# Performance work log

Hardware: AMD Instinct MI355X
Metric: run time of the kernel (lower is better)

## Reference

```python
import jax, jax.numpy as jnp
import numpy as np

B, N, D_IN = 256, 64, 128   # batch, n_agents, input_dim
H0, H1, H2 = 256, 256, 64   # rnn_hidden_dim[0], [1], [2]


def setup_inputs() -> dict:
    key = jax.random.key(0)
    ks = jax.random.split(key, 14)
    s = 0.05
    return {
        "obs": jax.random.normal(ks[0], (B, N, D_IN), dtype=jnp.float32),
        "W_enc": jax.random.normal(ks[1], (H0, D_IN), dtype=jnp.float32) * s,
        "b_enc": jax.random.normal(ks[2], (H0,), dtype=jnp.float32) * s,
        "W_obs": jax.random.normal(ks[3], (H0, H0), dtype=jnp.float32) * s,
        "b_obs": jax.random.normal(ks[4], (H0,), dtype=jnp.float32) * s,
        "W_ih": jax.random.normal(ks[5], (3 * H0, H0), dtype=jnp.float32) * s,
        "b_ih": jax.random.normal(ks[6], (3 * H0,), dtype=jnp.float32) * s,
        "W_hh": jax.random.normal(ks[7], (3 * H0, H0), dtype=jnp.float32) * s,
        "b_hh": jax.random.normal(ks[8], (3 * H0,), dtype=jnp.float32) * s,
        "W_val": jax.random.normal(ks[9], (H1, H0), dtype=jnp.float32) * s,
        "b_val": jax.random.normal(ks[10], (H1,), dtype=jnp.float32) * s,
        "W_dec": jax.random.normal(ks[11], (H2, H1), dtype=jnp.float32) * s,
        "b_dec": jax.random.normal(ks[12], (H2,), dtype=jnp.float32) * s,
    }


def reference(obs, W_enc, b_enc, W_obs, b_obs, W_ih, b_ih, W_hh, b_hh,
              W_val, b_val, W_dec, b_dec):
    # encoding + f_obs  -> h: [B, N, H0]
    x = jax.nn.relu(jnp.einsum("bnd,hd->bnh", obs, W_enc) + b_enc)
    h = jnp.einsum("bnh,gh->bng", x, W_obs) + b_obs

    # comm: mean over other agents. Original masks self and divides by N
    # (mean over dim of size N with self zeroed) => (sum_all - self) / N.
    c = (jnp.sum(h, axis=1, keepdims=True) - h) / N  # [B, N, H0]

    # GRUCell(input=c, hidden=h), PyTorch gate ordering r, z, n
    gi = jnp.einsum("bnh,gh->bng", c, W_ih) + b_ih   # [B, N, 3*H0]
    gh = jnp.einsum("bnh,gh->bng", h, W_hh) + b_hh
    gi_r, gi_z, gi_n = jnp.split(gi, 3, axis=-1)
    gh_r, gh_z, gh_n = jnp.split(gh, 3, axis=-1)
    r = jax.nn.sigmoid(gi_r + gh_r)
    z = jax.nn.sigmoid(gi_z + gh_z)
    n = jnp.tanh(gi_n + r * gh_n)
    h = (1.0 - z) * n + z * h  # [B, N, H0]

    # value head + decoding; seq_len=1 squeezed -> [B, N, H2]
    v = jnp.einsum("bnh,vh->bnv", h, W_val) + b_val
    out = jnp.einsum("bnv,ov->bno", v, W_dec) + b_dec
    return out
```

## Files before the change

### kernel.cpp

```cpp
#include <hip/hip_runtime.h>
#include <hip/hip_bf16.h>
#include <math.h>


typedef __bf16  bf16x8 __attribute__((ext_vector_type(8)));
typedef float   f32x4  __attribute__((ext_vector_type(4)));

#define DIN 128
#define H0  256
#define SW  264
#define SWO 136
#define LOG2E 1.44269504088896f

#define O_WENC 0
#define O_WOBS 32768
#define O_WIH  98304
#define O_WHH  294912
#define W_TOT4 491520
#define O_WVD  491520
#define BVD_BYTE 1015808

__device__ __forceinline__ f32x4 mfma16(bf16x8 a, bf16x8 b, f32x4 c) {
    return __builtin_amdgcn_mfma_f32_16x16x32_bf16(a, b, c, 0, 0, 0);
}
__device__ __forceinline__ float bf2f(__hip_bfloat16 x) { return __bfloat162float(x); }
__device__ __forceinline__ __hip_bfloat16 f2bf(float x) { return __float2bfloat16(x); }
__device__ __forceinline__ float fsigmoid(float x) {
    float e = __builtin_amdgcn_exp2f(-LOG2E * x);
    return __builtin_amdgcn_rcpf(1.0f + e);
}
__device__ __forceinline__ float ftanh(float x) {
    float e = __builtin_amdgcn_exp2f(2.0f * LOG2E * x);
    return 1.0f - 2.0f * __builtin_amdgcn_rcpf(1.0f + e);
}
__device__ __forceinline__ bf16x8 w8(const __hip_bfloat16* p, int idx) {
    return *(const bf16x8*)(p + idx);
}

__global__ __launch_bounds__(256) void prep_kernel(
    const float* __restrict__ W_enc, const float* __restrict__ W_obs,
    const float* __restrict__ W_ih,  const float* __restrict__ W_hh,
    __hip_bfloat16* __restrict__ ws)
{
    const int i = (blockIdx.x * 256 + threadIdx.x) * 8;
    if (i >= W_TOT4) return;
    const float* src; int off;
    if      (i < O_WOBS) { src = W_enc; off = O_WENC; }
    else if (i < O_WIH)  { src = W_obs; off = O_WOBS; }
    else if (i < O_WHH)  { src = W_ih;  off = O_WIH;  }
    else                 { src = W_hh;  off = O_WHH;  }
    const float* f = src + (i - off);
    f32x4 a = *(const f32x4*)f;
    f32x4 b = *(const f32x4*)(f + 4);
    bf16x8 v;
    #pragma unroll
    for (int j = 0; j < 4; j++) { v[j] = (__bf16)a[j]; v[j + 4] = (__bf16)b[j]; }
    *(bf16x8*)(ws + i) = v;
}

__global__ __launch_bounds__(256) void wvd_kernel(
    const float* __restrict__ W_dec, const float* __restrict__ W_val,
    const float* __restrict__ b_val, const float* __restrict__ b_dec,
    __hip_bfloat16* __restrict__ wvd, float* __restrict__ bvd)
{
    const int o = blockIdx.x;
    const int h = threadIdx.x;
    float acc = 0.0f;
    for (int v = 0; v < 256; v++)
        acc += W_dec[o * 256 + v] * W_val[v * 256 + h];
    wvd[o * 256 + h] = f2bf(acc);
    if (h == 0) {
        float b = b_dec[o];
        for (int v = 0; v < 256; v++) b += W_dec[o * 256 + v] * b_val[v];
        bvd[o] = b;
    }
}

__global__ __launch_bounds__(512, 1) void commnet_v8(
    const __hip_bfloat16* __restrict__ ws, const float* __restrict__ bvd,
    const float* __restrict__ b_enc, const float* __restrict__ b_obs,
    const float* __restrict__ b_ih,  const float* __restrict__ b_hh,
    const float* __restrict__ obs,   float* __restrict__ out)
{
    __shared__ __align__(16) __hip_bfloat16 T0[64 * SW];
    __shared__ __align__(16) __hip_bfloat16 T1[64 * SW];

    const __hip_bfloat16* W_enc = ws + O_WENC;
    const __hip_bfloat16* W_obs = ws + O_WOBS;
    const __hip_bfloat16* W_ih  = ws + O_WIH;
    const __hip_bfloat16* W_hh  = ws + O_WHH;
    const __hip_bfloat16* W_vd  = ws + O_WVD;

    const int tid  = threadIdx.x;
    const int wave = tid >> 6;
    const int lane = tid & 63;
    const int quad = lane >> 4;
    const int lc   = lane & 15;
    const int row0 = blockIdx.x * 64;
    const int ko16 = quad * 8;

    #pragma unroll
    for (int j = 0; j < 2; j++) {
        const int u = tid + j * 512;
        const int r = u >> 4, c = (u & 15) << 3;
        const float* src = obs + (row0 + r) * DIN + c;
        f32x4 a = *(const f32x4*)src;
        f32x4 b = *(const f32x4*)(src + 4);
        bf16x8 v;
        #pragma unroll
        for (int q = 0; q < 4; q++) { v[q] = (__bf16)a[q]; v[q + 4] = (__bf16)b[q]; }
        *(bf16x8*)&T1[r * SWO + c] = v;
    }
    __syncthreads();

    #pragma unroll
    for (int cp = 0; cp < 2; cp++) {
        const int n = (wave + 8 * cp) * 16 + lc;
        const float bias = b_enc[n];
        f32x4 acc[4] = {};
        bf16x8 wc = w8(W_enc, n * DIN + ko16);
        #pragma unroll
        for (int k0 = 0; k0 < DIN; k0 += 32) {
            bf16x8 wn = w8(W_enc, n * DIN + (((k0 + 32) & (DIN - 1)) + ko16));
            const int kk = k0 + ko16;
            #pragma unroll
            for (int rt = 0; rt < 4; rt++) {
                bf16x8 a = *(const bf16x8*)&T1[(rt * 16 + lc) * SWO + kk];
                acc[rt] = mfma16(a, wc, acc[rt]);
            }
            wc = wn;
        }
        #pragma unroll
        for (int rt = 0; rt < 4; rt++)
            #pragma unroll
            for (int i = 0; i < 4; i++)
                T0[(rt * 16 + quad * 4 + i) * SW + n] = f2bf(fmaxf(acc[rt][i] + bias, 0.0f));
    }
    __syncthreads();

    #pragma unroll
    for (int cp = 0; cp < 2; cp++) {
        const int n = (wave + 8 * cp) * 16 + lc;
        const float bias = b_obs[n];
        f32x4 acc[4] = {};
        bf16x8 wc = w8(W_obs, n * H0 + ko16);
        #pragma unroll 2
        for (int k0 = 0; k0 < H0; k0 += 32) {
            bf16x8 wn = w8(W_obs, n * H0 + (((k0 + 32) & (H0 - 1)) + ko16));
            const int kk = k0 + ko16;
            #pragma unroll
            for (int rt = 0; rt < 4; rt++) {
                bf16x8 a = *(const bf16x8*)&T0[(rt * 16 + lc) * SW + kk];
                acc[rt] = mfma16(a, wc, acc[rt]);
            }
            wc = wn;
        }
        #pragma unroll
        for (int rt = 0; rt < 4; rt++)
            #pragma unroll
            for (int i = 0; i < 4; i++)
                T1[(rt * 16 + quad * 4 + i) * SW + n] = f2bf(acc[rt][i] + bias);
    }
    __syncthreads();

    #pragma unroll
    for (int cp = 0; cp < 2; cp++) {
        const int n = (wave + 8 * cp) * 16 + lc;
        const float bir = b_ih[n], biz = b_ih[n + 256], bin = b_ih[n + 512];
        const float bhr = b_hh[n], bhz = b_hh[n + 256], bhn = b_hh[n + 512];
        f32x4 gir[4] = {}, giz[4] = {}, gin[4] = {};
        f32x4 ghr[4] = {}, ghz[4] = {}, ghn[4] = {};
        bf16x8 c0 = w8(W_ih, (n      ) * H0 + ko16);
        bf16x8 c1 = w8(W_ih, (n + 256) * H0 + ko16);
        bf16x8 c2 = w8(W_ih, (n + 512) * H0 + ko16);
        bf16x8 c3 = w8(W_hh, (n      ) * H0 + ko16);
        bf16x8 c4 = w8(W_hh, (n + 256) * H0 + ko16);
        bf16x8 c5 = w8(W_hh, (n + 512) * H0 + ko16);
        #pragma unroll 2
        for (int k0 = 0; k0 < H0; k0 += 32) {
            const int kn = ((k0 + 32) & (H0 - 1)) + ko16;
            bf16x8 d0 = w8(W_ih, (n      ) * H0 + kn);
            bf16x8 d1 = w8(W_ih, (n + 256) * H0 + kn);
            bf16x8 d2 = w8(W_ih, (n + 512) * H0 + kn);
            bf16x8 d3 = w8(W_hh, (n      ) * H0 + kn);
            bf16x8 d4 = w8(W_hh, (n + 256) * H0 + kn);
            bf16x8 d5 = w8(W_hh, (n + 512) * H0 + kn);
            const int kk = k0 + ko16;
            #pragma unroll
            for (int rt = 0; rt < 4; rt++) {
                bf16x8 aH = *(const bf16x8*)&T1[(rt * 16 + lc) * SW + kk];
                gir[rt] = mfma16(aH, c0, gir[rt]);
                giz[rt] = mfma16(aH, c1, giz[rt]);
                gin[rt] = mfma16(aH, c2, gin[rt]);
                ghr[rt] = mfma16(aH, c3, ghr[rt]);
                ghz[rt] = mfma16(aH, c4, ghz[rt]);
                ghn[rt] = mfma16(aH, c5, ghn[rt]);
            }
            c0 = d0; c1 = d1; c2 = d2; c3 = d3; c4 = d4; c5 = d5;
        }
        float Sr = 0.0f, Sz = 0.0f, Sn = 0.0f;
        #pragma unroll
        for (int rt = 0; rt < 4; rt++)
            #pragma unroll
            for (int i = 0; i < 4; i++) {
                Sr += gir[rt][i]; Sz += giz[rt][i]; Sn += gin[rt][i];
            }
        Sr += __shfl_xor(Sr, 16); Sr += __shfl_xor(Sr, 32);
        Sz += __shfl_xor(Sz, 16); Sz += __shfl_xor(Sz, 32);
        Sn += __shfl_xor(Sn, 16); Sn += __shfl_xor(Sn, 32);
        #pragma unroll
        for (int rt = 0; rt < 4; rt++)
            #pragma unroll
            for (int i = 0; i < 4; i++) {
                const int row = rt * 16 + quad * 4 + i;
                const float gi_r = (Sr - gir[rt][i]) * (1.0f / 64.0f) + bir;
                const float gi_z = (Sz - giz[rt][i]) * (1.0f / 64.0f) + biz;
                const float gi_n = (Sn - gin[rt][i]) * (1.0f / 64.0f) + bin;
                const float r  = fsigmoid(gi_r + ghr[rt][i] + bhr);
                const float z  = fsigmoid(gi_z + ghz[rt][i] + bhz);
                const float nn = ftanh(gi_n + r * (ghn[rt][i] + bhn));
                const float h  = bf2f(T1[row * SW + n]);
                T0[row * SW + n] = f2bf((1.0f - z) * nn + z * h);
            }
    }
    __syncthreads();

    {
        const int ct  = wave & 3;
        const int rtb = (wave >> 2) * 2;
        const int n   = ct * 16 + lc;
        const float bias = bvd[n];
        f32x4 acc[2] = {};
        bf16x8 wc = w8(W_vd, n * H0 + ko16);
        #pragma unroll
        for (int k0 = 0; k0 < H0; k0 += 32) {
            bf16x8 wn = w8(W_vd, n * H0 + (((k0 + 32) & (H0 - 1)) + ko16));
            const int kk = k0 + ko16;
            #pragma unroll
            for (int j = 0; j < 2; j++) {
                bf16x8 a = *(const bf16x8*)&T0[((rtb + j) * 16 + lc) * SW + kk];
                acc[j] = mfma16(a, wc, acc[j]);
            }
            wc = wn;
        }
        #pragma unroll
        for (int j = 0; j < 2; j++)
            #pragma unroll
            for (int i = 0; i < 4; i++) {
                const int row = (rtb + j) * 16 + quad * 4 + i;
                out[(row0 + row) * 64 + n] = acc[j][i] + bias;
            }
    }
}

extern "C" void kernel_launch(void* const* d_in, const int* in_sizes, int n_in,
                              void* d_out, int out_size, void* d_ws, size_t ws_size,
                              hipStream_t stream) {
    (void)in_sizes; (void)n_in; (void)out_size; (void)ws_size;
    const float* obs   = (const float*)d_in[0];
    const float* W_enc = (const float*)d_in[1];  const float* b_enc = (const float*)d_in[2];
    const float* W_obs = (const float*)d_in[3];  const float* b_obs = (const float*)d_in[4];
    const float* W_ih  = (const float*)d_in[5];  const float* b_ih  = (const float*)d_in[6];
    const float* W_hh  = (const float*)d_in[7];  const float* b_hh  = (const float*)d_in[8];
    const float* W_val = (const float*)d_in[9];  const float* b_val = (const float*)d_in[10];
    const float* W_dec = (const float*)d_in[11]; const float* b_dec = (const float*)d_in[12];
    float* out = (float*)d_out;
    __hip_bfloat16* ws = (__hip_bfloat16*)d_ws;
    float* bvd = (float*)((char*)d_ws + BVD_BYTE);

    prep_kernel<<<240, 256, 0, stream>>>(W_enc, W_obs, W_ih, W_hh, ws);
    wvd_kernel<<<64, 256, 0, stream>>>(W_dec, W_val, b_val, b_dec, ws + O_WVD, bvd);
    commnet_v8<<<256, 512, 0, stream>>>(ws, bvd, b_enc, b_obs, b_ih, b_hh, obs, out);
}
```

Baseline: 134.7 us.

## Use 1024-thread blocks, split GRU gates into two passes, merge prep kernels

The main kernel now runs 16 waves per block, so each wave owns one 16-column slice instead of looping over two. The GRU stage is split into an r/z pass and an n pass, which lowers the live accumulator count per wave; r is staged in LDS as bf16 and z is kept in registers. The prep and W_val·W_dec fold kernels are merged into one launch, and the fold loop gets four independent accumulators. The split adds a second read of the hidden state from LDS per gate pass, drops the weight prefetch double-buffering, and rounds r to bf16, which costs a little precision.

```diff
diff --git a/kernel.cpp b/kernel.cpp
--- a/kernel.cpp
+++ b/kernel.cpp
@@ -40,43 +40,52 @@
 __global__ __launch_bounds__(256) void prep_kernel(
     const float* __restrict__ W_enc, const float* __restrict__ W_obs,
     const float* __restrict__ W_ih,  const float* __restrict__ W_hh,
-    __hip_bfloat16* __restrict__ ws)
+    const float* __restrict__ W_val, const float* __restrict__ W_dec,
+    const float* __restrict__ b_val, const float* __restrict__ b_dec,
+    __hip_bfloat16* __restrict__ ws, float* __restrict__ bvd)
 {
-    const int i = (blockIdx.x * 256 + threadIdx.x) * 8;
-    if (i >= W_TOT4) return;
-    const float* src; int off;
-    if      (i < O_WOBS) { src = W_enc; off = O_WENC; }
-    else if (i < O_WIH)  { src = W_obs; off = O_WOBS; }
-    else if (i < O_WHH)  { src = W_ih;  off = O_WIH;  }
-    else                 { src = W_hh;  off = O_WHH;  }
-    const float* f = src + (i - off);
-    f32x4 a = *(const f32x4*)f;
-    f32x4 b = *(const f32x4*)(f + 4);
-    bf16x8 v;
-    #pragma unroll
-    for (int j = 0; j < 4; j++) { v[j] = (__bf16)a[j]; v[j + 4] = (__bf16)b[j]; }
-    *(bf16x8*)(ws + i) = v;
-}
-
-__global__ __launch_bounds__(256) void wvd_kernel(
-    const float* __restrict__ W_dec, const float* __restrict__ W_val,
-    const float* __restrict__ b_val, const float* __restrict__ b_dec,
-    __hip_bfloat16* __restrict__ wvd, float* __restrict__ bvd)
-{
-    const int o = blockIdx.x;
-    const int h = threadIdx.x;
-    float acc = 0.0f;
-    for (int v = 0; v < 256; v++)
-        acc += W_dec[o * 256 + v] * W_val[v * 256 + h];
-    wvd[o * 256 + h] = f2bf(acc);
-    if (h == 0) {
-        float b = b_dec[o];
-        for (int v = 0; v < 256; v++) b += W_dec[o * 256 + v] * b_val[v];
-        bvd[o] = b;
-    }
-}
-
-__global__ __launch_bounds__(512, 1) void commnet_v8(
+    if (blockIdx.x < 240) {
+        const int i = (blockIdx.x * 256 + threadIdx.x) * 8;
+        const float* src; int off;
+        if      (i < O_WOBS) { src = W_enc; off = O_WENC; }
+        else if (i < O_WIH)  { src = W_obs; off = O_WOBS; }
+        else if (i < O_WHH)  { src = W_ih;  off = O_WIH;  }
+        else                 { src = W_hh;  off = O_WHH;  }
+        const float* f = src + (i - off);
+        f32x4 a = *(const f32x4*)f;
+        f32x4 b = *(const f32x4*)(f + 4);
+        bf16x8 v;
+        #pragma unroll
+        for (int j = 0; j < 4; j++) { v[j] = (__bf16)a[j]; v[j + 4] = (__bf16)b[j]; }
+        *(bf16x8*)(ws + i) = v;
+    } else {
+        const int o = blockIdx.x - 240;
+        const int h = threadIdx.x;
+        const float* wd = W_dec + o * 256;
+        float a0 = 0.f, a1 = 0.f, a2 = 0.f, a3 = 0.f;
+        for (int v4 = 0; v4 < 64; v4++) {
+            const int v = v4 * 4;
+            a0 += wd[v    ] * W_val[(v    ) * 256 + h];
+            a1 += wd[v + 1] * W_val[(v + 1) * 256 + h];
+            a2 += wd[v + 2] * W_val[(v + 2) * 256 + h];
+            a3 += wd[v + 3] * W_val[(v + 3) * 256 + h];
+        }
+        ws[O_WVD + o * 256 + h] = f2bf((a0 + a1) + (a2 + a3));
+        if (h == 0) {
+            float b0 = 0.f, b1 = 0.f, b2 = 0.f, b3 = 0.f;
+            for (int v4 = 0; v4 < 64; v4++) {
+                const int v = v4 * 4;
+                b0 += wd[v] * b_val[v];     b1 += wd[v + 1] * b_val[v + 1];
+                b2 += wd[v + 2] * b_val[v + 2]; b3 += wd[v + 3] * b_val[v + 3];
+            }
+            bvd[o] = b_dec[o] + (b0 + b1) + (b2 + b3);
+        }
+    }
+}
+
+__global__ __attribute__((amdgpu_flat_work_group_size(1024, 1024),
+                          amdgpu_waves_per_eu(4, 4)))
+void commnet_v9(
     const __hip_bfloat16* __restrict__ ws, const float* __restrict__ bvd,
     const float* __restrict__ b_enc, const float* __restrict__ b_obs,
     const float* __restrict__ b_ih,  const float* __restrict__ b_hh,
@@ -98,11 +107,10 @@
     const int lc   = lane & 15;
     const int row0 = blockIdx.x * 64;
     const int ko16 = quad * 8;
-
-    #pragma unroll
-    for (int j = 0; j < 2; j++) {
-        const int u = tid + j * 512;
-        const int r = u >> 4, c = (u & 15) << 3;
+    const int n    = wave * 16 + lc;
+
+    {
+        const int r = tid >> 4, c = (tid & 15) << 3;
         const float* src = obs + (row0 + r) * DIN + c;
         f32x4 a = *(const f32x4*)src;
         f32x4 b = *(const f32x4*)(src + 4);
@@ -113,9 +121,7 @@
     }
     __syncthreads();
 
-    #pragma unroll
-    for (int cp = 0; cp < 2; cp++) {
-        const int n = (wave + 8 * cp) * 16 + lc;
+    {
         const float bias = b_enc[n];
         f32x4 acc[4] = {};
         bf16x8 wc = w8(W_enc, n * DIN + ko16);
@@ -138,9 +144,7 @@
     }
     __syncthreads();
 
-    #pragma unroll
-    for (int cp = 0; cp < 2; cp++) {
-        const int n = (wave + 8 * cp) * 16 + lc;
+    {
         const float bias = b_obs[n];
         f32x4 acc[4] = {};
         bf16x8 wc = w8(W_obs, n * H0 + ko16);
@@ -163,51 +167,34 @@
     }
     __syncthreads();
 
-    #pragma unroll
-    for (int cp = 0; cp < 2; cp++) {
-        const int n = (wave + 8 * cp) * 16 + lc;
-        const float bir = b_ih[n], biz = b_ih[n + 256], bin = b_ih[n + 512];
-        const float bhr = b_hh[n], bhz = b_hh[n + 256], bhn = b_hh[n + 512];
-        f32x4 gir[4] = {}, giz[4] = {}, gin[4] = {};
-        f32x4 ghr[4] = {}, ghz[4] = {}, ghn[4] = {};
-        bf16x8 c0 = w8(W_ih, (n      ) * H0 + ko16);
-        bf16x8 c1 = w8(W_ih, (n + 256) * H0 + ko16);
-        bf16x8 c2 = w8(W_ih, (n + 512) * H0 + ko16);
-        bf16x8 c3 = w8(W_hh, (n      ) * H0 + ko16);
-        bf16x8 c4 = w8(W_hh, (n + 256) * H0 + ko16);
-        bf16x8 c5 = w8(W_hh, (n + 512) * H0 + ko16);
-        #pragma unroll 2
-        for (int k0 = 0; k0 < H0; k0 += 32) {
-            const int kn = ((k0 + 32) & (H0 - 1)) + ko16;
-            bf16x8 d0 = w8(W_ih, (n      ) * H0 + kn);
-            bf16x8 d1 = w8(W_ih, (n + 256) * H0 + kn);
-            bf16x8 d2 = w8(W_ih, (n + 512) * H0 + kn);
-            bf16x8 d3 = w8(W_hh, (n      ) * H0 + kn);
-            bf16x8 d4 = w8(W_hh, (n + 256) * H0 + kn);
-            bf16x8 d5 = w8(W_hh, (n + 512) * H0 + kn);
-            const int kk = k0 + ko16;
+    f32x4 zreg[4];
+    {
+        const float bir = b_ih[n], biz = b_ih[n + 256];
+        const float bhr = b_hh[n], bhz = b_hh[n + 256];
+        f32x4 gir[4] = {}, giz[4] = {}, ghr[4] = {}, ghz[4] = {};
+        #pragma unroll 2
+        for (int k0 = 0; k0 < H0; k0 += 32) {
+            const int kk = k0 + ko16;
+            bf16x8 c0 = w8(W_ih, (n      ) * H0 + kk);
+            bf16x8 c1 = w8(W_ih, (n + 256) * H0 + kk);
+            bf16x8 c3 = w8(W_hh, (n      ) * H0 + kk);
+            bf16x8 c4 = w8(W_hh, (n + 256) * H0 + kk);
             #pragma unroll
             for (int rt = 0; rt < 4; rt++) {
                 bf16x8 aH = *(const bf16x8*)&T1[(rt * 16 + lc) * SW + kk];
                 gir[rt] = mfma16(aH, c0, gir[rt]);
                 giz[rt] = mfma16(aH, c1, giz[rt]);
-                gin[rt] = mfma16(aH, c2, gin[rt]);
                 ghr[rt] = mfma16(aH, c3, ghr[rt]);
                 ghz[rt] = mfma16(aH, c4, ghz[rt]);
-                ghn[rt] = mfma16(aH, c5, ghn[rt]);
-            }
-            c0 = d0; c1 = d1; c2 = d2; c3 = d3; c4 = d4; c5 = d5;
-        }
-        float Sr = 0.0f, Sz = 0.0f, Sn = 0.0f;
-        #pragma unroll
-        for (int rt = 0; rt < 4; rt++)
-            #pragma unroll
-            for (int i = 0; i < 4; i++) {
-                Sr += gir[rt][i]; Sz += giz[rt][i]; Sn += gin[rt][i];
-            }
+            }
+        }
+        float Sr = 0.0f, Sz = 0.0f;
+        #pragma unroll
+        for (int rt = 0; rt < 4; rt++)
+            #pragma unroll
+            for (int i = 0; i < 4; i++) { Sr += gir[rt][i]; Sz += giz[rt][i]; }
         Sr += __shfl_xor(Sr, 16); Sr += __shfl_xor(Sr, 32);
         Sz += __shfl_xor(Sz, 16); Sz += __shfl_xor(Sz, 32);
-        Sn += __shfl_xor(Sn, 16); Sn += __shfl_xor(Sn, 32);
         #pragma unroll
         for (int rt = 0; rt < 4; rt++)
             #pragma unroll
@@ -215,10 +202,40 @@
                 const int row = rt * 16 + quad * 4 + i;
                 const float gi_r = (Sr - gir[rt][i]) * (1.0f / 64.0f) + bir;
                 const float gi_z = (Sz - giz[rt][i]) * (1.0f / 64.0f) + biz;
+                T0[row * SW + n] = f2bf(fsigmoid(gi_r + ghr[rt][i] + bhr));
+                zreg[rt][i]      = fsigmoid(gi_z + ghz[rt][i] + bhz);
+            }
+    }
+    {
+        const float bin = b_ih[n + 512], bhn = b_hh[n + 512];
+        f32x4 gin[4] = {}, ghn[4] = {};
+        #pragma unroll 2
+        for (int k0 = 0; k0 < H0; k0 += 32) {
+            const int kk = k0 + ko16;
+            bf16x8 c2 = w8(W_ih, (n + 512) * H0 + kk);
+            bf16x8 c5 = w8(W_hh, (n + 512) * H0 + kk);
+            #pragma unroll
+            for (int rt = 0; rt < 4; rt++) {
+                bf16x8 aH = *(const bf16x8*)&T1[(rt * 16 + lc) * SW + kk];
+                gin[rt] = mfma16(aH, c2, gin[rt]);
+                ghn[rt] = mfma16(aH, c5, ghn[rt]);
+            }
+        }
+        float Sn = 0.0f;
+        #pragma unroll
+        for (int rt = 0; rt < 4; rt++)
+            #pragma unroll
+            for (int i = 0; i < 4; i++) Sn += gin[rt][i];
+        Sn += __shfl_xor(Sn, 16); Sn += __shfl_xor(Sn, 32);
+        #pragma unroll
+        for (int rt = 0; rt < 4; rt++)
+            #pragma unroll
+            for (int i = 0; i < 4; i++) {
+                const int row = rt * 16 + quad * 4 + i;
                 const float gi_n = (Sn - gin[rt][i]) * (1.0f / 64.0f) + bin;
-                const float r  = fsigmoid(gi_r + ghr[rt][i] + bhr);
-                const float z  = fsigmoid(gi_z + ghz[rt][i] + bhz);
-                const float nn = ftanh(gi_n + r * (ghn[rt][i] + bhn));
+                const float rr = bf2f(T0[row * SW + n]);
+                const float nn = ftanh(gi_n + rr * (ghn[rt][i] + bhn));
+                const float z  = zreg[rt][i];
                 const float h  = bf2f(T1[row * SW + n]);
                 T0[row * SW + n] = f2bf((1.0f - z) * nn + z * h);
             }
@@ -226,30 +243,25 @@
     __syncthreads();
 
     {
-        const int ct  = wave & 3;
-        const int rtb = (wave >> 2) * 2;
-        const int n   = ct * 16 + lc;
-        const float bias = bvd[n];
-        f32x4 acc[2] = {};
-        bf16x8 wc = w8(W_vd, n * H0 + ko16);
-        #pragma unroll
-        for (int k0 = 0; k0 < H0; k0 += 32) {
-            bf16x8 wn = w8(W_vd, n * H0 + (((k0 + 32) & (H0 - 1)) + ko16));
-            const int kk = k0 + ko16;
-            #pragma unroll
-            for (int j = 0; j < 2; j++) {
-                bf16x8 a = *(const bf16x8*)&T0[((rtb + j) * 16 + lc) * SW + kk];
-                acc[j] = mfma16(a, wc, acc[j]);
-            }
+        const int ct = wave & 3;
+        const int rg = wave >> 2;
+        const int nd = ct * 16 + lc;
+        const float bias = bvd[nd];
+        f32x4 acc = {};
+        bf16x8 wc = w8(W_vd, nd * H0 + ko16);
+        #pragma unroll 2
+        for (int k0 = 0; k0 < H0; k0 += 32) {
+            bf16x8 wn = w8(W_vd, nd * H0 + (((k0 + 32) & (H0 - 1)) + ko16));
+            const int kk = k0 + ko16;
+            bf16x8 a = *(const bf16x8*)&T0[(rg * 16 + lc) * SW + kk];
+            acc = mfma16(a, wc, acc);
             wc = wn;
         }
         #pragma unroll
-        for (int j = 0; j < 2; j++)
-            #pragma unroll
-            for (int i = 0; i < 4; i++) {
-                const int row = (rtb + j) * 16 + quad * 4 + i;
-                out[(row0 + row) * 64 + n] = acc[j][i] + bias;
-            }
+        for (int i = 0; i < 4; i++) {
+            const int row = rg * 16 + quad * 4 + i;
+            out[(row0 + row) * 64 + nd] = acc[i] + bias;
+        }
     }
 }
 
@@ -268,7 +280,7 @@
     __hip_bfloat16* ws = (__hip_bfloat16*)d_ws;
     float* bvd = (float*)((char*)d_ws + BVD_BYTE);
 
-    prep_kernel<<<240, 256, 0, stream>>>(W_enc, W_obs, W_ih, W_hh, ws);
-    wvd_kernel<<<64, 256, 0, stream>>>(W_dec, W_val, b_val, b_dec, ws + O_WVD, bvd);
-    commnet_v8<<<256, 512, 0, stream>>>(ws, bvd, b_enc, b_obs, b_ih, b_hh, obs, out);
-}
+    prep_kernel<<<304, 256, 0, stream>>>(W_enc, W_obs, W_ih, W_hh,
+                                         W_val, W_dec, b_val, b_dec, ws, bvd);
+    commnet_v9<<<256, 1024, 0, stream>>>(ws, bvd, b_enc, b_obs, b_ih, b_hh, obs, out);
+}
```

Result: faster. 127.8 us (-5.1%).
